# Kernel tuning notes

Hardware: AMD Instinct MI355X
Metric: run time of the kernel (lower is better)

The kernel has to match this reference:

```python
import jax, jax.numpy as jnp
import numpy as np
from jax import lax

B, C1, H, W = 4, 256, 160, 160
C = 128        # hidden c = int(c2 * e)
C2 = 256
GC = 512
NG = 16        # number of guide embeddings
K = int(H * W * 0.007)  # 179 top pixels per image


def _conv(x, w, b, act):
    # ultralytics Conv = Conv2d + BN + SiLU; BN (eval) folded into conv bias.
    y = lax.conv_general_dilated(x, w, (1, 1), 'SAME', dimension_numbers=('NCHW', 'OIHW', 'NCHW'))
    y = y + b[None, :, None, None]
    return y * jax.nn.sigmoid(y) if act else y


def setup_inputs():
    key = jax.random.key(0)
    ks = jax.random.split(key, 16)
    rn = lambda k, s, sc=1.0: jax.random.normal(k, s, dtype=jnp.float32) * sc
    z = lambda n: jnp.zeros((n,), jnp.float32)
    return {
        'x': rn(ks[0], (B, C1, H, W)),
        'guide': rn(ks[1], (B, NG, GC)),
        'cv1_w': rn(ks[2], (2 * C, C1, 1, 1), (1.0 / C1) ** 0.5),
        'cv1_b': z(2 * C),
        'm1_w': rn(ks[3], (C, C, 3, 3), (1.0 / (C * 9)) ** 0.5),
        'm1_b': z(C),
        'm2_w': rn(ks[4], (C, C, 3, 3), (1.0 / (C * 9)) ** 0.5),
        'm2_b': z(C),
        'gl_w': rn(ks[5], (C, GC), (1.0 / GC) ** 0.5),
        'gl_b': z(C),
        'attn_bias': z(1),
        'proj_w': rn(ks[6], (C, C, 3, 3), (1.0 / (C * 9)) ** 0.5),
        'proj_b': z(C),
        'cv2_w': rn(ks[7], (C2, 4 * C, 1, 1), (1.0 / (4 * C)) ** 0.5),
        'cv2_b': z(C2),
        'gcn1_w': rn(ks[8], (C2, 64), (1.0 / C2) ** 0.5),
        'gcn1_b': z(64),
        'gcn2_w': rn(ks[9], (64, C2), (1.0 / 64) ** 0.5),
        'gcn2_b': z(C2),
    }


def reference(x, guide, cv1_w, cv1_b, m1_w, m1_b, m2_w, m2_b, gl_w, gl_b, attn_bias, proj_w, proj_b, cv2_w, cv2_b, gcn1_w, gcn1_b, gcn2_w, gcn2_b):
    bs, _, h, w = x.shape
    y0 = _conv(x, cv1_w, cv1_b, True)
    a, b = y0[:, :C], y0[:, C:]
    # Bottleneck(shortcut=False, e=1.0): two 3x3 Convs, no residual add
    m_out = _conv(_conv(b, m1_w, m1_b, True), m2_w, m2_b, True)
    # ScoreCompute: nh=1, hc=C, c1==ec so no ec conv, scale=1.0
    g = guide @ gl_w.T + gl_b                      # (bs, NG, C)
    aw = jnp.einsum('bchw,bnc->bhwn', m_out, g)    # nh==1 collapses bmchw,bnmc->bmhwn
    aw = jnp.max(aw, axis=-1) / (C ** 0.5) + attn_bias[0]
    aw = jax.nn.sigmoid(aw)                        # (bs, h, w); score == aw since nh == 1
    new = _conv(m_out, proj_w, proj_b, False) * aw[:, None]
    z = _conv(jnp.concatenate([a, b, m_out, new], axis=1), cv2_w, cv2_b, True)
    # --- top-K pixel gather per image ---
    _, idx = lax.top_k(aw.reshape(bs, -1), K)      # (bs, K)
    flat_z = z.reshape(bs, C2, h * w)
    feats = jnp.take_along_axis(flat_z, idx[:, None, :], axis=2)  # (bs, C2, K)
    X = feats.transpose(0, 2, 1).reshape(bs * K, C2)
    # --- dynamic cosine-similarity graph (dense adjacency form of nonzero edge list) ---
    nf = X / jnp.maximum(jnp.linalg.norm(X, axis=1, keepdims=True), 1e-12)
    A = (nf @ nf.T > 0.5).astype(X.dtype)          # diagonal always present (self-sim = 1)
    A_hat = A + jnp.eye(bs * K, dtype=X.dtype)     # GCNConv adds its own self-loops
    dinv = 1.0 / jnp.sqrt(jnp.sum(A_hat, axis=1))
    An = dinv[:, None] * A_hat * dinv[None, :]     # D^-1/2 (A+I) D^-1/2
    h1 = jax.nn.relu(An @ (X @ gcn1_w) + gcn1_b)
    upd = An @ (h1 @ gcn2_w) + gcn2_b              # (bs*K, C2)
    upd = upd.reshape(bs, K, C2).transpose(0, 2, 1)
    # --- scatter updated node features back into the dense map ---
    out = flat_z.at[jnp.arange(bs)[:, None, None], jnp.arange(C2)[None, :, None], idx[:, None, :]].set(upd)
    return out.reshape(bs, C2, h, w)
```

## Files before the change

### kernel.cpp

```cpp
#include <hip/hip_runtime.h>
#include <math.h>

#define HW 25600
#define Wd 160
#define Hd 160
#define Bsz 4
#define Cc 128
#define Kk 179

__device__ __forceinline__ float silu_f(float y){ return y / (1.0f + expf(-y)); }

__device__ __forceinline__ int xcd_swizzle(int flat, int nblk) {
    return (nblk >> 3) * (flat & 7) + (flat >> 3);
}

__global__ __launch_bounds__(256) void cv1_kernel(
    const float* __restrict__ x, const float* __restrict__ w,
    const float* __restrict__ bias, float* __restrict__ y0)
{
    const int flat = blockIdx.x + 16 * (blockIdx.y + 25 * blockIdx.z);
    const int wk = xcd_swizzle(flat, 1600);
    const int cog = wk & 15;
    const int rest = wk >> 4;
    const int pxb = rest % 25;
    const int b = rest / 25;

    const int t = threadIdx.x;
    const int p0 = pxb * 1024 + t * 4;
    const int co0 = cog * 16;
    const float* xb = x + (size_t)b * 256 * HW + p0;
    float4 acc[16];
#pragma unroll
    for (int k = 0; k < 16; ++k) acc[k] = make_float4(0.f, 0.f, 0.f, 0.f);

    for (int ci0 = 0; ci0 < 256; ci0 += 4) {
        float4 v[4];
#pragma unroll
        for (int j = 0; j < 4; ++j)
            v[j] = *(const float4*)(xb + (size_t)(ci0 + j) * HW);
#pragma unroll
        for (int co = 0; co < 16; ++co) {
            const float* wr = w + (size_t)(co0 + co) * 256 + ci0;
#pragma unroll
            for (int j = 0; j < 4; ++j) {
                float wv = wr[j];
                acc[co].x = fmaf(wv, v[j].x, acc[co].x);
                acc[co].y = fmaf(wv, v[j].y, acc[co].y);
                acc[co].z = fmaf(wv, v[j].z, acc[co].z);
                acc[co].w = fmaf(wv, v[j].w, acc[co].w);
            }
        }
    }
#pragma unroll
    for (int co = 0; co < 16; ++co) {
        float bv = bias[co0 + co];
        float4 a = acc[co];
        a.x = silu_f(a.x + bv); a.y = silu_f(a.y + bv);
        a.z = silu_f(a.z + bv); a.w = silu_f(a.w + bv);
        *(float4*)(y0 + ((size_t)b * 256 + co0 + co) * HW + p0) = a;
    }
}

__global__ __launch_bounds__(256) void conv3x3_kernel(
    const float* __restrict__ in, long in_bstride,
    const float* __restrict__ w, const float* __restrict__ bias,
    float* __restrict__ out, long out_bstride,
    const float* __restrict__ awp, int act)
{
    const int flat = blockIdx.x + 8 * (blockIdx.y + 25 * blockIdx.z);
    const int wk = xcd_swizzle(flat, 800);
    const int cog = wk & 7;
    const int rest = wk >> 3;
    const int tile = rest % 25;
    const int b = rest / 25;

    const int tid = threadIdx.x;
    const int ty = tid >> 3;
    const int tx0 = (tid & 7) * 4;
    const int x0 = (tile % 5) * 32;
    const int y0_ = (tile / 5) * 32;
    const int co0 = cog * 16;
    const int oy = y0_ + ty, ox = x0 + tx0;

    const float* inb = in + (size_t)b * in_bstride;

    int rb[3]; float mrow[3];
#pragma unroll
    for (int r = 0; r < 3; ++r) {
        int gy = oy + r - 1;
        mrow[r] = (gy >= 0 && gy < Hd) ? 1.f : 0.f;
        int gyc = gy < 0 ? 0 : (gy > Hd - 1 ? Hd - 1 : gy);
        rb[r] = gyc * Wd;
    }
    const float mc0 = (ox - 1 >= 0) ? 1.f : 0.f;
    const float mc5 = (ox + 4 < Wd) ? 1.f : 0.f;
    const int c0 = (ox - 1 >= 0) ? ox - 1 : 0;
    const int c5 = (ox + 4 < Wd) ? ox + 4 : Wd - 1;

    float4 acc[16];
#pragma unroll
    for (int k = 0; k < 16; ++k) acc[k] = make_float4(0.f, 0.f, 0.f, 0.f);

    for (int ci = 0; ci < 128; ++ci) {
        const float* pc = inb + (size_t)ci * HW;
        float win[18];
#pragma unroll
        for (int r = 0; r < 3; ++r) {
            const float* rp = pc + rb[r];
            float4 mid = *(const float4*)(rp + ox);
            float mm = mrow[r];
            win[r * 6 + 0] = rp[c0] * (mm * mc0);
            win[r * 6 + 1] = mid.x * mm;
            win[r * 6 + 2] = mid.y * mm;
            win[r * 6 + 3] = mid.z * mm;
            win[r * 6 + 4] = mid.w * mm;
            win[r * 6 + 5] = rp[c5] * (mm * mc5);
        }
        const float* wc = w + ((size_t)co0 * 128 + ci) * 9;
#pragma unroll
        for (int co = 0; co < 16; ++co) {
            const float* wr = wc + (size_t)co * 128 * 9;
#pragma unroll
            for (int t = 0; t < 9; ++t) {
                const int dy = t / 3, dx = t % 3;
                float wv = wr[t];
                acc[co].x = fmaf(wv, win[dy * 6 + dx + 0], acc[co].x);
                acc[co].y = fmaf(wv, win[dy * 6 + dx + 1], acc[co].y);
                acc[co].z = fmaf(wv, win[dy * 6 + dx + 2], acc[co].z);
                acc[co].w = fmaf(wv, win[dy * 6 + dx + 3], acc[co].w);
            }
        }
    }

    float4 awv = make_float4(1.f, 1.f, 1.f, 1.f);
    if (awp) awv = *(const float4*)(awp + b * HW + oy * Wd + ox);
#pragma unroll
    for (int co = 0; co < 16; ++co) {
        float bv = bias[co0 + co];
        float4 a = acc[co];
        a.x += bv; a.y += bv; a.z += bv; a.w += bv;
        if (act) {
            a.x = silu_f(a.x); a.y = silu_f(a.y);
            a.z = silu_f(a.z); a.w = silu_f(a.w);
        } else {
            a.x *= awv.x; a.y *= awv.y; a.z *= awv.z; a.w *= awv.w;
        }
        *(float4*)(out + (size_t)b * out_bstride + (size_t)(co0 + co) * HW + oy * Wd + ox) = a;
    }
}

__global__ void g_kernel(const float* __restrict__ guide, const float* __restrict__ glw,
                         const float* __restrict__ glb, float* __restrict__ g)
{
    const int bn = blockIdx.x;
    const int c = threadIdx.x;
    const float* gr = guide + (size_t)bn * 512;
    const float* wr = glw + (size_t)c * 512;
    float acc = 0.f;
    for (int k = 0; k < 512; ++k) acc += gr[k] * wr[k];
    g[bn * 128 + c] = acc + glb[c];
}

__global__ __launch_bounds__(256) void attn_kernel(
    const float* __restrict__ mo, const float* __restrict__ g,
    const float* __restrict__ ab, float* __restrict__ aw)
{
    const int p = blockIdx.x * 256 + threadIdx.x;
    const int b = blockIdx.y;
    __shared__ float gl[128 * 16];
    for (int l = threadIdx.x; l < 2048; l += 256) {
        int n = l & 15, c = l >> 4;
        gl[l] = g[(b * 16 + n) * 128 + c];
    }
    __syncthreads();
    float acc[16];
#pragma unroll
    for (int n = 0; n < 16; ++n) acc[n] = 0.f;
    const float* mb = mo + (size_t)b * 128 * HW + p;
    for (int c = 0; c < 128; ++c) {
        float v = mb[(size_t)c * HW];
        const float4* g4 = (const float4*)(&gl[c * 16]);
#pragma unroll
        for (int n4 = 0; n4 < 4; ++n4) {
            float4 gv = g4[n4];
            acc[n4 * 4 + 0] += v * gv.x;
            acc[n4 * 4 + 1] += v * gv.y;
            acc[n4 * 4 + 2] += v * gv.z;
            acc[n4 * 4 + 3] += v * gv.w;
        }
    }
    float m = acc[0];
#pragma unroll
    for (int n = 1; n < 16; ++n) m = fmaxf(m, acc[n]);
    float logit = m / sqrtf(128.f) + ab[0];
    aw[b * HW + p] = 1.f / (1.f + expf(-logit));
}

__global__ __launch_bounds__(256) void cv2_kernel(
    const float* __restrict__ y0, const float* __restrict__ mo, const float* __restrict__ nw,
    const float* __restrict__ w, const float* __restrict__ bias, float* __restrict__ out)
{
    const int flat = blockIdx.x + 16 * (blockIdx.y + 25 * blockIdx.z);
    const int wk = xcd_swizzle(flat, 1600);
    const int cog = wk & 15;
    const int rest = wk >> 4;
    const int pxb = rest % 25;
    const int b = rest / 25;

    const int t = threadIdx.x;
    const int p0 = pxb * 1024 + t * 4;
    const int co0 = cog * 16;
    float4 acc[16];
#pragma unroll
    for (int k = 0; k < 16; ++k) acc[k] = make_float4(0.f, 0.f, 0.f, 0.f);

    for (int blk = 0; blk < 4; ++blk) {
        const float* src;
        if (blk == 0)      src = y0 + (size_t)b * 256 * HW;
        else if (blk == 1) src = y0 + ((size_t)b * 256 + 128) * HW;
        else if (blk == 2) src = mo + (size_t)b * 128 * HW;
        else               src = nw + (size_t)b * 128 * HW;
        src += p0;
        for (int ci0 = 0; ci0 < 128; ci0 += 4) {
            float4 v[4];
#pragma unroll
            for (int j = 0; j < 4; ++j)
                v[j] = *(const float4*)(src + (size_t)(ci0 + j) * HW);
#pragma unroll
            for (int co = 0; co < 16; ++co) {
                const float* wr = w + (size_t)(co0 + co) * 512 + blk * 128 + ci0;
#pragma unroll
                for (int j = 0; j < 4; ++j) {
                    float wv = wr[j];
                    acc[co].x = fmaf(wv, v[j].x, acc[co].x);
                    acc[co].y = fmaf(wv, v[j].y, acc[co].y);
                    acc[co].z = fmaf(wv, v[j].z, acc[co].z);
                    acc[co].w = fmaf(wv, v[j].w, acc[co].w);
                }
            }
        }
    }
#pragma unroll
    for (int co = 0; co < 16; ++co) {
        float bv = bias[co0 + co];
        float4 a = acc[co];
        a.x = silu_f(a.x + bv); a.y = silu_f(a.y + bv);
        a.z = silu_f(a.z + bv); a.w = silu_f(a.w + bv);
        *(float4*)(out + ((size_t)b * 256 + co0 + co) * HW + p0) = a;
    }
}

__global__ __launch_bounds__(1024) void topk_kernel(
    const float* __restrict__ aw, int* __restrict__ idx, int* __restrict__ ties)
{
    const int b = blockIdx.x;
    const float* v = aw + b * HW;
    __shared__ unsigned hist[256];
    __shared__ unsigned s_sel;
    __shared__ int s_rem;
    __shared__ int s_cnt, s_tcnt;
    const int tid = threadIdx.x;
    unsigned prefix = 0; int rem = Kk;
    for (int shift = 24; shift >= 0; shift -= 8) {
        if (tid < 256) hist[tid] = 0;
        __syncthreads();
        unsigned mask_hi = (shift == 24) ? 0u : ~((1u << (shift + 8)) - 1u);
        for (int i = tid; i < HW; i += 1024) {
            unsigned u = __float_as_uint(v[i]);
            if ((u & mask_hi) == (prefix & mask_hi))
                atomicAdd(&hist[(u >> shift) & 255], 1u);
        }
        __syncthreads();
        if (tid == 0) {
            int cum = 0; unsigned bsel = 0;
            for (int xq = 255; xq >= 0; --xq) {
                int h = (int)hist[xq];
                if (cum + h >= rem) { bsel = (unsigned)xq; break; }
                cum += h;
            }
            s_sel = bsel; s_rem = rem - cum;
        }
        __syncthreads();
        prefix |= (s_sel << shift);
        rem = s_rem;
        __syncthreads();
    }
    const unsigned T = prefix;
    if (tid == 0) { s_cnt = 0; s_tcnt = 0; }
    __syncthreads();
    for (int i = tid; i < HW; i += 1024) {
        unsigned u = __float_as_uint(v[i]);
        if (u > T)       { int p = atomicAdd(&s_cnt, 1);  idx[b * Kk + p] = i; }
        else if (u == T) { int p = atomicAdd(&s_tcnt, 1); ties[b * HW + p] = i; }
    }
    __syncthreads();
    if (tid == 0) {
        int base = s_cnt;
        int need = Kk - base;
        int tn = s_tcnt;
        int* tb = ties + b * HW;
        for (int s = 0; s < need; ++s) {
            int mn = 0x7fffffff, mi = -1;
            for (int t = 0; t < tn; ++t) if (tb[t] < mn) { mn = tb[t]; mi = t; }
            idx[b * Kk + base + s] = mn;
            if (mi >= 0) tb[mi] = 0x7fffffff;
        }
    }
}

__global__ __launch_bounds__(256) void gather_kernel(
    const float* __restrict__ z, const int* __restrict__ idx,
    float* __restrict__ X, float* __restrict__ ninv)
{
    const int m = blockIdx.x;
    const int b = m / Kk;
    const int pix = idx[m];
    const int c = threadIdx.x;
    float v = z[((size_t)b * 256 + c) * HW + pix];
    X[(size_t)m * 256 + c] = v;
    float s = v * v;
#pragma unroll
    for (int o = 32; o; o >>= 1) s += __shfl_down(s, o, 64);
    __shared__ float red[4];
    if ((c & 63) == 0) red[c >> 6] = s;
    __syncthreads();
    if (c == 0) {
        float t = red[0] + red[1] + red[2] + red[3];
        float nr = sqrtf(t);
        ninv[m] = 1.f / fmaxf(nr, 1e-12f);
    }
}

__global__ __launch_bounds__(256) void adj_kernel(
    const float* __restrict__ X, const float* __restrict__ ninv,
    float* __restrict__ Ah, float* __restrict__ dinv)
{
    const int i = blockIdx.x;
    const int tid = threadIdx.x;
    __shared__ float Xi[256];
    Xi[tid] = X[(size_t)i * 256 + tid];
    __syncthreads();
    const float ni = ninv[i];
    float rs = 0.f;
    for (int j = tid; j < 716; j += 256) {
        const float* Xj = X + (size_t)j * 256;
        float d = 0.f;
        for (int c = 0; c < 256; ++c) d += Xi[c] * Xj[c];
        float s = d * ni * ninv[j];
        float ah = (s > 0.5f) ? 1.f : 0.f;
        if (j == i) ah += 1.f;
        Ah[(size_t)i * 716 + j] = ah;
        rs += ah;
    }
#pragma unroll
    for (int o = 32; o; o >>= 1) rs += __shfl_down(rs, o, 64);
    __shared__ float red[4];
    if ((tid & 63) == 0) red[tid >> 6] = rs;
    __syncthreads();
    if (tid == 0) {
        float t = red[0] + red[1] + red[2] + red[3];
        dinv[i] = 1.f / sqrtf(t);
    }
}

__global__ void y1_kernel(const float* __restrict__ X, const float* __restrict__ w1,
                          float* __restrict__ Y1)
{
    const int i = blockIdx.x, co = threadIdx.x;
    const float* Xi = X + (size_t)i * 256;
    float acc = 0.f;
    for (int c = 0; c < 256; ++c) acc += Xi[c] * w1[c * 64 + co];
    Y1[i * 64 + co] = acc;
}

__global__ void h1_kernel(const float* __restrict__ Ah, const float* __restrict__ dinv,
                          const float* __restrict__ Y1, const float* __restrict__ b1,
                          float* __restrict__ h1)
{
    const int i = blockIdx.x, co = threadIdx.x;
    float acc = 0.f;
    const float* Ar = Ah + (size_t)i * 716;
    for (int j = 0; j < 716; ++j) {
        float a = Ar[j];
        if (a != 0.f) acc += a * dinv[j] * Y1[j * 64 + co];
    }
    float vv = dinv[i] * acc + b1[co];
    h1[i * 64 + co] = fmaxf(vv, 0.f);
}

__global__ void y2_kernel(const float* __restrict__ h1, const float* __restrict__ w2,
                          float* __restrict__ Y2)
{
    const int i = blockIdx.x, co = threadIdx.x;
    const float* hi = h1 + (size_t)i * 64;
    float acc = 0.f;
    for (int c = 0; c < 64; ++c) acc += hi[c] * w2[c * 256 + co];
    Y2[i * 256 + co] = acc;
}

__global__ void upd_kernel(const float* __restrict__ Ah, const float* __restrict__ dinv,
                           const float* __restrict__ Y2, const float* __restrict__ b2,
                           const int* __restrict__ idx, float* __restrict__ out)
{
    const int i = blockIdx.x, co = threadIdx.x;
    const int b = i / Kk;
    const int pix = idx[i];
    float acc = 0.f;
    const float* Ar = Ah + (size_t)i * 716;
    for (int j = 0; j < 716; ++j) {
        float a = Ar[j];
        if (a != 0.f) acc += a * dinv[j] * Y2[(size_t)j * 256 + co];
    }
    out[((size_t)b * 256 + co) * HW + pix] = dinv[i] * acc + b2[co];
}

extern "C" void kernel_launch(void* const* d_in, const int* in_sizes, int n_in,
                              void* d_out, int out_size, void* d_ws, size_t ws_size,
                              hipStream_t stream) {
    const float* x     = (const float*)d_in[0];
    const float* guide = (const float*)d_in[1];
    const float* cv1w  = (const float*)d_in[2];
    const float* cv1b  = (const float*)d_in[3];
    const float* m1w   = (const float*)d_in[4];
    const float* m1b   = (const float*)d_in[5];
    const float* m2w   = (const float*)d_in[6];
    const float* m2b   = (const float*)d_in[7];
    const float* glw   = (const float*)d_in[8];
    const float* glb   = (const float*)d_in[9];
    const float* attb  = (const float*)d_in[10];
    const float* pw    = (const float*)d_in[11];
    const float* pb    = (const float*)d_in[12];
    const float* c2w   = (const float*)d_in[13];
    const float* c2b   = (const float*)d_in[14];
    const float* g1w   = (const float*)d_in[15];
    const float* g1b   = (const float*)d_in[16];
    const float* g2w   = (const float*)d_in[17];
    const float* g2b   = (const float*)d_in[18];
    float* out = (float*)d_out;

    char* ws = (char*)d_ws;
    size_t off = 0;
    auto alloc = [&](size_t bytes) -> void* {
        void* p = ws + off;
        off += (bytes + 255) & ~(size_t)255;
        return p;
    };
    float* y0   = (float*)alloc(sizeof(float) * (size_t)Bsz * 256 * HW);
    float* t1   = (float*)alloc(sizeof(float) * (size_t)Bsz * 128 * HW);
    float* mo   = (float*)alloc(sizeof(float) * (size_t)Bsz * 128 * HW);
    float* aw   = (float*)alloc(sizeof(float) * Bsz * HW);
    float* g    = (float*)alloc(sizeof(float) * 64 * 128);
    float* X    = (float*)alloc(sizeof(float) * 716 * 256);
    float* ninv = (float*)alloc(sizeof(float) * 716);
    float* Ah   = (float*)alloc(sizeof(float) * 716 * 716);
    float* dinv = (float*)alloc(sizeof(float) * 716);
    float* Y1   = (float*)alloc(sizeof(float) * 716 * 64);
    float* h1v  = (float*)alloc(sizeof(float) * 716 * 64);
    float* Y2   = (float*)alloc(sizeof(float) * 716 * 256);
    int* idx    = (int*)alloc(sizeof(int) * 716);
    int* ties   = (int*)alloc(sizeof(int) * (size_t)Bsz * HW);

    g_kernel<<<dim3(64), dim3(128), 0, stream>>>(guide, glw, glb, g);
    cv1_kernel<<<dim3(16, 25, 4), dim3(256), 0, stream>>>(x, cv1w, cv1b, y0);
    conv3x3_kernel<<<dim3(8, 25, 4), dim3(256), 0, stream>>>(
        y0 + (size_t)128 * HW, (long)256 * HW, m1w, m1b, t1, (long)128 * HW, nullptr, 1);
    conv3x3_kernel<<<dim3(8, 25, 4), dim3(256), 0, stream>>>(
        t1, (long)128 * HW, m2w, m2b, mo, (long)128 * HW, nullptr, 1);
    attn_kernel<<<dim3(100, 4), dim3(256), 0, stream>>>(mo, g, attb, aw);
    conv3x3_kernel<<<dim3(8, 25, 4), dim3(256), 0, stream>>>(
        mo, (long)128 * HW, pw, pb, t1, (long)128 * HW, aw, 0);
    cv2_kernel<<<dim3(16, 25, 4), dim3(256), 0, stream>>>(y0, mo, t1, c2w, c2b, out);
    topk_kernel<<<dim3(4), dim3(1024), 0, stream>>>(aw, idx, ties);
    gather_kernel<<<dim3(716), dim3(256), 0, stream>>>(out, idx, X, ninv);
    adj_kernel<<<dim3(716), dim3(256), 0, stream>>>(X, ninv, Ah, dinv);
    y1_kernel<<<dim3(716), dim3(64), 0, stream>>>(X, g1w, Y1);
    h1_kernel<<<dim3(716), dim3(64), 0, stream>>>(Ah, dinv, Y1, g1b, h1v);
    y2_kernel<<<dim3(716), dim3(256), 0, stream>>>(h1v, g2w, Y2);
    upd_kernel<<<dim3(716), dim3(256), 0, stream>>>(Ah, dinv, Y2, g2b, idx, out);
}
```

Measured before the change: 2.039 ms.

## Transpose conv weights to ci-major layout and vectorize attention over four pixels

Adds small transpose kernels that rewrite the cv1, cv2 and 3x3 conv weights into input-channel-major order. The conv kernels can then read a thread's 16 output-channel weights contiguously, which allows wider scalar/vector loads in place of strided ones. The attention kernel now handles four pixels per thread with float4 loads, which cuts the block count and reuses each shared guide value across four pixels. This costs five extra small kernel launches per call and more accumulator registers in the attention kernel.

```diff
diff --git a/kernel.cpp b/kernel.cpp
--- a/kernel.cpp
+++ b/kernel.cpp
@@ -14,8 +14,24 @@
     return (nblk >> 3) * (flat & 7) + (flat >> 3);
 }
 
+__global__ void wtr_mat_kernel(const float* __restrict__ w, float* __restrict__ wt,
+                               int nco, int nci)
+{
+    const int ci = blockIdx.x;
+    const int co = threadIdx.x;
+    wt[(size_t)ci * nco + co] = w[(size_t)co * nci + ci];
+}
+__global__ void wtr3_kernel(const float* __restrict__ w, float* __restrict__ wt)
+{
+    const int ci = blockIdx.x;
+    const int co = threadIdx.x;
+#pragma unroll
+    for (int t = 0; t < 9; ++t)
+        wt[((size_t)ci * 128 + co) * 9 + t] = w[((size_t)co * 128 + ci) * 9 + t];
+}
+
 __global__ __launch_bounds__(256) void cv1_kernel(
-    const float* __restrict__ x, const float* __restrict__ w,
+    const float* __restrict__ x, const float* __restrict__ wt,
     const float* __restrict__ bias, float* __restrict__ y0)
 {
     const int flat = blockIdx.x + 16 * (blockIdx.y + 25 * blockIdx.z);
@@ -39,11 +55,11 @@
         for (int j = 0; j < 4; ++j)
             v[j] = *(const float4*)(xb + (size_t)(ci0 + j) * HW);
 #pragma unroll
-        for (int co = 0; co < 16; ++co) {
-            const float* wr = w + (size_t)(co0 + co) * 256 + ci0;
-#pragma unroll
-            for (int j = 0; j < 4; ++j) {
-                float wv = wr[j];
+        for (int j = 0; j < 4; ++j) {
+            const float* wr = wt + (size_t)(ci0 + j) * 256 + co0;
+#pragma unroll
+            for (int co = 0; co < 16; ++co) {
+                float wv = wr[co];
                 acc[co].x = fmaf(wv, v[j].x, acc[co].x);
                 acc[co].y = fmaf(wv, v[j].y, acc[co].y);
                 acc[co].z = fmaf(wv, v[j].z, acc[co].z);
@@ -63,7 +79,7 @@
 
 __global__ __launch_bounds__(256) void conv3x3_kernel(
     const float* __restrict__ in, long in_bstride,
-    const float* __restrict__ w, const float* __restrict__ bias,
+    const float* __restrict__ wt, const float* __restrict__ bias,
     float* __restrict__ out, long out_bstride,
     const float* __restrict__ awp, int act)
 {
@@ -116,10 +132,10 @@
             win[r * 6 + 4] = mid.w * mm;
             win[r * 6 + 5] = rp[c5] * (mm * mc5);
         }
-        const float* wc = w + ((size_t)co0 * 128 + ci) * 9;
+        const float* wc = wt + ((size_t)ci * 128 + co0) * 9;
 #pragma unroll
         for (int co = 0; co < 16; ++co) {
-            const float* wr = wc + (size_t)co * 128 * 9;
+            const float* wr = wc + co * 9;
 #pragma unroll
             for (int t = 0; t < 9; ++t) {
                 const int dy = t / 3, dx = t % 3;
@@ -165,7 +181,7 @@
     const float* __restrict__ mo, const float* __restrict__ g,
     const float* __restrict__ ab, float* __restrict__ aw)
 {
-    const int p = blockIdx.x * 256 + threadIdx.x;
+    const int p0 = blockIdx.x * 1024 + threadIdx.x * 4;
     const int b = blockIdx.y;
     __shared__ float gl[128 * 16];
     for (int l = threadIdx.x; l < 2048; l += 256) {
@@ -173,32 +189,48 @@
         gl[l] = g[(b * 16 + n) * 128 + c];
     }
     __syncthreads();
-    float acc[16];
-#pragma unroll
-    for (int n = 0; n < 16; ++n) acc[n] = 0.f;
-    const float* mb = mo + (size_t)b * 128 * HW + p;
+    float4 acc[16];
+#pragma unroll
+    for (int n = 0; n < 16; ++n) acc[n] = make_float4(0.f, 0.f, 0.f, 0.f);
+    const float* mb = mo + (size_t)b * 128 * HW + p0;
     for (int c = 0; c < 128; ++c) {
-        float v = mb[(size_t)c * HW];
+        float4 v = *(const float4*)(mb + (size_t)c * HW);
         const float4* g4 = (const float4*)(&gl[c * 16]);
 #pragma unroll
         for (int n4 = 0; n4 < 4; ++n4) {
             float4 gv = g4[n4];
-            acc[n4 * 4 + 0] += v * gv.x;
-            acc[n4 * 4 + 1] += v * gv.y;
-            acc[n4 * 4 + 2] += v * gv.z;
-            acc[n4 * 4 + 3] += v * gv.w;
-        }
-    }
-    float m = acc[0];
-#pragma unroll
-    for (int n = 1; n < 16; ++n) m = fmaxf(m, acc[n]);
-    float logit = m / sqrtf(128.f) + ab[0];
-    aw[b * HW + p] = 1.f / (1.f + expf(-logit));
+#pragma unroll
+            for (int q = 0; q < 4; ++q) {
+                float gw = (q == 0) ? gv.x : (q == 1) ? gv.y : (q == 2) ? gv.z : gv.w;
+                float4& a = acc[n4 * 4 + q];
+                a.x = fmaf(gw, v.x, a.x);
+                a.y = fmaf(gw, v.y, a.y);
+                a.z = fmaf(gw, v.z, a.z);
+                a.w = fmaf(gw, v.w, a.w);
+            }
+        }
+    }
+    float4 m = acc[0];
+#pragma unroll
+    for (int n = 1; n < 16; ++n) {
+        m.x = fmaxf(m.x, acc[n].x);
+        m.y = fmaxf(m.y, acc[n].y);
+        m.z = fmaxf(m.z, acc[n].z);
+        m.w = fmaxf(m.w, acc[n].w);
+    }
+    const float s = 1.f / sqrtf(128.f);
+    const float bb = ab[0];
+    float4 r;
+    r.x = 1.f / (1.f + expf(-(m.x * s + bb)));
+    r.y = 1.f / (1.f + expf(-(m.y * s + bb)));
+    r.z = 1.f / (1.f + expf(-(m.z * s + bb)));
+    r.w = 1.f / (1.f + expf(-(m.w * s + bb)));
+    *(float4*)(aw + b * HW + p0) = r;
 }
 
 __global__ __launch_bounds__(256) void cv2_kernel(
     const float* __restrict__ y0, const float* __restrict__ mo, const float* __restrict__ nw,
-    const float* __restrict__ w, const float* __restrict__ bias, float* __restrict__ out)
+    const float* __restrict__ wt, const float* __restrict__ bias, float* __restrict__ out)
 {
     const int flat = blockIdx.x + 16 * (blockIdx.y + 25 * blockIdx.z);
     const int wk = xcd_swizzle(flat, 1600);
@@ -227,11 +259,11 @@
             for (int j = 0; j < 4; ++j)
                 v[j] = *(const float4*)(src + (size_t)(ci0 + j) * HW);
 #pragma unroll
-            for (int co = 0; co < 16; ++co) {
-                const float* wr = w + (size_t)(co0 + co) * 512 + blk * 128 + ci0;
-#pragma unroll
-                for (int j = 0; j < 4; ++j) {
-                    float wv = wr[j];
+            for (int j = 0; j < 4; ++j) {
+                const float* wr = wt + (size_t)(blk * 128 + ci0 + j) * 256 + co0;
+#pragma unroll
+                for (int co = 0; co < 16; ++co) {
+                    float wv = wr[co];
                     acc[co].x = fmaf(wv, v[j].x, acc[co].x);
                     acc[co].y = fmaf(wv, v[j].y, acc[co].y);
                     acc[co].z = fmaf(wv, v[j].z, acc[co].z);
@@ -459,17 +491,28 @@
     float* Y2   = (float*)alloc(sizeof(float) * 716 * 256);
     int* idx    = (int*)alloc(sizeof(int) * 716);
     int* ties   = (int*)alloc(sizeof(int) * (size_t)Bsz * HW);
+    float* wt1  = (float*)alloc(sizeof(float) * 256 * 256);
+    float* wt2  = (float*)alloc(sizeof(float) * 512 * 256);
+    float* wtm1 = (float*)alloc(sizeof(float) * 128 * 128 * 9);
+    float* wtm2 = (float*)alloc(sizeof(float) * 128 * 128 * 9);
+    float* wtp  = (float*)alloc(sizeof(float) * 128 * 128 * 9);
+
+    wtr_mat_kernel<<<dim3(256), dim3(256), 0, stream>>>(cv1w, wt1, 256, 256);
+    wtr_mat_kernel<<<dim3(512), dim3(256), 0, stream>>>(c2w, wt2, 256, 512);
+    wtr3_kernel<<<dim3(128), dim3(128), 0, stream>>>(m1w, wtm1);
+    wtr3_kernel<<<dim3(128), dim3(128), 0, stream>>>(m2w, wtm2);
+    wtr3_kernel<<<dim3(128), dim3(128), 0, stream>>>(pw, wtp);
 
     g_kernel<<<dim3(64), dim3(128), 0, stream>>>(guide, glw, glb, g);
-    cv1_kernel<<<dim3(16, 25, 4), dim3(256), 0, stream>>>(x, cv1w, cv1b, y0);
+    cv1_kernel<<<dim3(16, 25, 4), dim3(256), 0, stream>>>(x, wt1, cv1b, y0);
     conv3x3_kernel<<<dim3(8, 25, 4), dim3(256), 0, stream>>>(
-        y0 + (size_t)128 * HW, (long)256 * HW, m1w, m1b, t1, (long)128 * HW, nullptr, 1);
+        y0 + (size_t)128 * HW, (long)256 * HW, wtm1, m1b, t1, (long)128 * HW, nullptr, 1);
     conv3x3_kernel<<<dim3(8, 25, 4), dim3(256), 0, stream>>>(
-        t1, (long)128 * HW, m2w, m2b, mo, (long)128 * HW, nullptr, 1);
-    attn_kernel<<<dim3(100, 4), dim3(256), 0, stream>>>(mo, g, attb, aw);
+        t1, (long)128 * HW, wtm2, m2b, mo, (long)128 * HW, nullptr, 1);
+    attn_kernel<<<dim3(25, 4), dim3(256), 0, stream>>>(mo, g, attb, aw);
     conv3x3_kernel<<<dim3(8, 25, 4), dim3(256), 0, stream>>>(
-        mo, (long)128 * HW, pw, pb, t1, (long)128 * HW, aw, 0);
-    cv2_kernel<<<dim3(16, 25, 4), dim3(256), 0, stream>>>(y0, mo, t1, c2w, c2b, out);
+        mo, (long)128 * HW, wtp, pb, t1, (long)128 * HW, aw, 0);
+    cv2_kernel<<<dim3(16, 25, 4), dim3(256), 0, stream>>>(y0, mo, t1, wt2, c2b, out);
     topk_kernel<<<dim3(4), dim3(1024), 0, stream>>>(aw, idx, ties);
     gather_kernel<<<dim3(716), dim3(256), 0, stream>>>(out, idx, X, ninv);
     adj_kernel<<<dim3(716), dim3(256), 0, stream>>>(X, ninv, Ah, dinv);
```

Measured after the change: 1.993 ms. -2.2%, faster.
